# Optimization experiments

Measured on AMD Instinct MI355X. Metric: run time of the kernel, lower is better.

## Reference

```python
import jax, jax.numpy as jnp
import numpy as np

B, S, HID = 1, 2048, 1024
HQ, HKV, D = 16, 8, 64
W = 64          # causal window size (includes self at offset 0)
K = 128         # total neighbors per query: W window + (K-W) random rewires


def setup_inputs() -> dict:
    key = jax.random.key(0)
    ks = jax.random.split(key, 8)
    hidden_states = jax.random.normal(ks[0], (B, S, HID), jnp.float32)
    sc = HID ** -0.5
    q_w = jax.random.normal(ks[1], (HQ * D, HID), jnp.float32) * sc
    k_w = jax.random.normal(ks[2], (HKV * D, HID), jnp.float32) * sc
    v_w = jax.random.normal(ks[3], (HKV * D, HID), jnp.float32) * sc
    o_w = jax.random.normal(ks[4], (HQ * D, HID), jnp.float32).T * sc  # [HID, HQ*D] -> stored as [HID, HQ*D]? keep [HID, HQ*D]
    o_w = jax.random.normal(ks[4], (HID, HQ * D), jnp.float32) * sc
    edge_bias = jax.random.normal(ks[5], (4,), jnp.float32) * 0.1
    # neighbor indices: per kv-head, per query position.
    pos = jnp.arange(S)
    win = pos[:, None] - jnp.arange(W)[None, :]                    # [S, W], offset 0 == self
    win = jnp.broadcast_to(win[None], (HKV, S, W))
    rew = jax.random.randint(ks[6], (HKV, S, K - W), 0, S)         # random rewire edges
    neigh_idx = jnp.concatenate([win, rew], axis=-1).astype(jnp.int32)  # [HKV, S, K]
    edge_type = jnp.concatenate([
        jnp.full((HKV, S, W), 1, jnp.int32),       # 'window'
        jnp.full((HKV, S, K - W), 3, jnp.int32),   # 'rewire'
    ], axis=-1)
    return {
        'hidden_states': hidden_states, 'q_w': q_w, 'k_w': k_w, 'v_w': v_w,
        'o_w': o_w, 'edge_bias': edge_bias, 'neigh_idx': neigh_idx,
        'edge_type': edge_type,
    }


def reference(hidden_states, q_w, k_w, v_w, o_w, edge_bias, neigh_idx, edge_type):
    b, s, _ = hidden_states.shape
    hkv, _, kk = neigh_idx.shape
    hq = q_w.shape[0] // (k_w.shape[0] // hkv)
    d = k_w.shape[0] // hkv
    hq = q_w.shape[0] // d
    g = hq // hkv
    scaling = d ** -0.5

    # projections (nn.Linear: x @ W.T)
    q = (hidden_states @ q_w.T).reshape(b, s, hq, d).transpose(0, 2, 1, 3)    # [B,HQ,S,D]
    k = (hidden_states @ k_w.T).reshape(b, s, hkv, d).transpose(0, 2, 1, 3)   # [B,HKV,S,D]
    v = (hidden_states @ v_w.T).reshape(b, s, hkv, d).transpose(0, 2, 1, 3)

    # causal neighbor mask + safe clamp (mirrors _causal_neighbor_mask / _safe_neighbor_idx)
    pos = jnp.arange(s)
    mask = (neigh_idx >= 0) & (neigh_idx < s) & (neigh_idx <= pos[None, :, None])  # [HKV,S,K]
    safe = jnp.clip(neigh_idx, 0, s - 1)

    # gather K/V at neighbor indices: [B,HKV,S,K,D]
    h_idx = jnp.arange(hkv)[:, None, None]
    k_g = k[:, h_idx, safe, :]
    v_g = v[:, h_idx, safe, :]

    # GQA: group query heads over kv heads
    qg = q.reshape(b, hkv, g, s, d)
    scores = jnp.einsum('bhgsd,bhskd->bhgsk', qg, k_g) * scaling              # [B,HKV,G,S,K]
    scores = scores + edge_bias[edge_type][None, :, None, :, :]
    neg = jnp.finfo(scores.dtype).min
    scores = jnp.where(mask[None, :, None, :, :], scores, neg)
    attn = jax.nn.softmax(scores, axis=-1)

    out = jnp.einsum('bhgsk,bhskd->bhgsd', attn, v_g)                         # [B,HKV,G,S,D]
    out = out.reshape(b, hq, s, d).transpose(0, 2, 1, 3).reshape(b, s, hq * d)
    return out @ o_w.T                                                        # [B,S,HID]
```

## Files before the change

kernel.cpp:

```cpp
#include <hip/hip_runtime.h>
#include <hip/hip_bf16.h>

#define S_LEN 2048
#define HIDDEN 1024

typedef __attribute__((ext_vector_type(4))) float f32x4;
typedef __attribute__((ext_vector_type(8))) _Float16 f16x8;
typedef __attribute__((ext_vector_type(2))) _Float16 f16x2;
typedef __attribute__((ext_vector_type(2))) __fp16 fp16x2;
typedef unsigned short u16;
typedef unsigned int u32;

typedef const __attribute__((address_space(1))) unsigned int as1_u32;
typedef __attribute__((address_space(3))) unsigned int as3_u32;

__device__ __forceinline__ u16 f2h(float f) {
  union { _Float16 h; u16 u; } c; c.h = (_Float16)f; return c.u;
}
__device__ __forceinline__ f16x2 u2h2(u32 u) {
  union { u32 x; f16x2 h; } c; c.x = u; return c.h;
}
__device__ __forceinline__ float fdot2(u32 a, u32 b, float c) {
#if __has_builtin(__builtin_amdgcn_fdot2)
  return __builtin_amdgcn_fdot2(u2h2(a), u2h2(b), c, false);
#else
  f16x2 ha = u2h2(a), hb = u2h2(b);
  return fmaf((float)ha.x, (float)hb.x, fmaf((float)ha.y, (float)hb.y, c));
#endif
}
__device__ __forceinline__ u32 pkrtz(float a, float b) {
#if __has_builtin(__builtin_amdgcn_cvt_pkrtz)
  union { fp16x2 h; u32 u; } c;
  c.h = __builtin_amdgcn_cvt_pkrtz(a, b);
  return c.u;
#else
  union { f16x2 h; u32 u; } c;
  c.h.x = (_Float16)a; c.h.y = (_Float16)b;
  return c.u;
#endif
}

__global__ __launch_bounds__(256) void cvt_all(
    const float* __restrict__ h, const float* __restrict__ qw,
    const float* __restrict__ kw, const float* __restrict__ vw,
    const float* __restrict__ ow, u16* __restrict__ hb, u16* __restrict__ qwb,
    u16* __restrict__ kwb, u16* __restrict__ vwb, u16* __restrict__ owb) {
  const int b = blockIdx.x;
  const float* src; u16* dst; int base;
  if (b < 2048)      { src = h;  dst = hb;  base = b; }
  else if (b < 3072) { src = qw; dst = qwb; base = b - 2048; }
  else if (b < 3584) { src = kw; dst = kwb; base = b - 3072; }
  else if (b < 4096) { src = vw; dst = vwb; base = b - 3584; }
  else               { src = ow; dst = owb; base = b - 4096; }
  const int i = base * 256 + threadIdx.x;
  const float4 v = ((const float4*)src)[i];
  ushort4 r;
  r.x = f2h(v.x); r.y = f2h(v.y); r.z = f2h(v.z); r.w = f2h(v.w);
  ((ushort4*)dst)[i] = r;
}

template <int BM, bool OUT_F16>
__device__ __forceinline__ void gemm_core(
    u16* __restrict__ As, u16* __restrict__ Bs,
    const u16* __restrict__ A, const u16* __restrict__ W, void* __restrict__ Cv,
    int Kd, int ldc, int mtile, int ntile) {
  constexpr int MF = BM / 32;
  const int tid = threadIdx.x;
  const int lane = tid & 63;
  const int wave = tid >> 6;
  const int wr = wave >> 1, wc = wave & 1;
  f32x4 acc[MF][4] = {};
  const int m0 = mtile * BM, n0 = ntile * 128;

  for (int kt = 0; kt < Kd; kt += 32) {
#pragma unroll
    for (int i = 0; i < BM / 64; ++i) {
      const int e = (i * 256 + tid) * 8;
      const int r = e >> 5, c = e & 31;
      __builtin_amdgcn_global_load_lds(
          (as1_u32*)(A + (size_t)(m0 + r) * Kd + kt + c), (as3_u32*)(As + e), 16, 0, 0);
    }
#pragma unroll
    for (int i = 0; i < 2; ++i) {
      const int e = (i * 256 + tid) * 8;
      const int r = e >> 5, c = e & 31;
      __builtin_amdgcn_global_load_lds(
          (as1_u32*)(W + (size_t)(n0 + r) * Kd + kt + c), (as3_u32*)(Bs + e), 16, 0, 0);
    }
    __syncthreads();
    f16x8 af[MF], bfr[4];
#pragma unroll
    for (int mi = 0; mi < MF; ++mi)
      af[mi] = *(const f16x8*)(As + (wr * (BM / 2) + mi * 16 + (lane & 15)) * 32 + (lane >> 4) * 8);
#pragma unroll
    for (int ni = 0; ni < 4; ++ni)
      bfr[ni] = *(const f16x8*)(Bs + (wc * 64 + ni * 16 + (lane & 15)) * 32 + (lane >> 4) * 8);
#pragma unroll
    for (int mi = 0; mi < MF; ++mi)
#pragma unroll
      for (int ni = 0; ni < 4; ++ni)
        acc[mi][ni] = __builtin_amdgcn_mfma_f32_16x16x32_f16(af[mi], bfr[ni], acc[mi][ni], 0, 0, 0);
    __syncthreads();
  }

#pragma unroll
  for (int mi = 0; mi < MF; ++mi) {
#pragma unroll
    for (int ni = 0; ni < 4; ++ni) {
      const int row0 = m0 + wr * (BM / 2) + mi * 16 + (lane >> 4) * 4;
      const int col = n0 + wc * 64 + ni * 16 + (lane & 15);
#pragma unroll
      for (int r = 0; r < 4; ++r) {
        if (OUT_F16)
          ((u16*)Cv)[(size_t)(row0 + r) * ldc + col] = f2h(acc[mi][ni][r]);
        else
          ((float*)Cv)[(size_t)(row0 + r) * ldc + col] = acc[mi][ni][r];
      }
    }
  }
}

__global__ __launch_bounds__(256, 2) void qkv_gemm(
    const u16* __restrict__ hb, const u16* __restrict__ qwb,
    const u16* __restrict__ kwb, const u16* __restrict__ vwb,
    u16* __restrict__ Qb, u16* __restrict__ Kb, u16* __restrict__ Vb) {
  __shared__ u16 As[128 * 32];
  __shared__ u16 Bs[128 * 32];
  const int nt = blockIdx.x, mt = blockIdx.y;
  if (nt < 8)       gemm_core<128, true>(As, Bs, hb, qwb, Qb, HIDDEN, 1024, mt, nt);
  else if (nt < 12) gemm_core<128, true>(As, Bs, hb, kwb, Kb, HIDDEN, 512, mt, nt - 8);
  else              gemm_core<128, true>(As, Bs, hb, vwb, Vb, HIDDEN, 512, mt, nt - 12);
}

__global__ __launch_bounds__(256, 2) void o_gemm(
    const u16* __restrict__ attnb, const u16* __restrict__ owb,
    float* __restrict__ out) {
  __shared__ u16 As[64 * 32];
  __shared__ u16 Bs[128 * 32];
  gemm_core<64, false>(As, Bs, attnb, owb, out, HIDDEN, 1024, blockIdx.y, blockIdx.x);
}

#define WIN_ROWS 72
#define WIN_ELEMS (WIN_ROWS * 64)
__global__ __launch_bounds__(256, 5) void attn_kernel(
    const u16* __restrict__ Qb, const u16* __restrict__ Kb,
    const u16* __restrict__ Vb, const int* __restrict__ neigh,
    const float* __restrict__ ebias, u16* __restrict__ attnb) {
  __shared__ u16 kwin[WIN_ELEMS];
  __shared__ u16 vwin[WIN_ELEMS];
  __shared__ u32 park[4][192];

  const int tid = threadIdx.x;
  const int lane = tid & 63;
  const int wv = tid >> 6;
  const int h = blockIdx.y;
  const int s0 = blockIdx.x * 4;
  const int s = s0 + wv;

  const u16* Kp = Kb + h * 64;
  const u16* Vp = Vb + h * 64;

  const int iB = neigh[((size_t)h * S_LEN + s) * 128 + 64 + lane];
  const bool okB = (iB >= 0) && (iB <= s);
  const int gB = min(max(iB, 0), S_LEN - 1);
  const bool okA = lane <= s;

  const u16* krp = Kp + (size_t)gB * 512;
  uint4 krreg[8];
#pragma unroll
  for (int t = 0; t < 8; ++t) krreg[t] = *(const uint4*)(krp + t * 8);

  const int chunk = (lane & 7) ^ (lane >> 3);
#pragma unroll
  for (int gg = 0; gg < 2; ++gg) {
    const int g = wv + gg * 4;
    const int r_lds = g * 8 + (lane >> 3);
    const int row = min(max(s0 - 63 + r_lds, 0), S_LEN - 1);
    __builtin_amdgcn_global_load_lds(
        (as1_u32*)(Kp + (size_t)row * 512 + chunk * 8),
        (as3_u32*)(kwin + g * 512 + lane * 8), 16, 0, 0);
    __builtin_amdgcn_global_load_lds(
        (as1_u32*)(Vp + (size_t)row * 512 + chunk * 8),
        (as3_u32*)(vwin + g * 512 + lane * 8), 16, 0, 0);
  }
  if (wv == 0) {
    const int g = 8;
    const int r_lds = g * 8 + (lane >> 3);
    const int row = min(max(s0 - 63 + r_lds, 0), S_LEN - 1);
    __builtin_amdgcn_global_load_lds(
        (as1_u32*)(Kp + (size_t)row * 512 + chunk * 8),
        (as3_u32*)(kwin + g * 512 + lane * 8), 16, 0, 0);
    __builtin_amdgcn_global_load_lds(
        (as1_u32*)(Vp + (size_t)row * 512 + chunk * 8),
        (as3_u32*)(vwin + g * 512 + lane * 8), 16, 0, 0);
  }

  __syncthreads();

  const u16* qp = Qb + (size_t)s * 1024 + h * 128;
  const int rW = wv + 63 - lane;
  const u16* kwrow = kwin + rW * 64;
  const int rw7 = rW & 7;
  float sA0 = 0.f, sA1 = 0.f, sB0 = 0.f, sB1 = 0.f;
#pragma unroll
  for (int t = 0; t < 8; ++t) {
    const uint4 kw = *(const uint4*)(kwrow + ((t ^ rw7) << 3));
    const uint4 kr = krreg[t];
    const uint4 qa = *(const uint4*)(qp + t * 8);
    const uint4 qb = *(const uint4*)(qp + 64 + t * 8);
    sA0 = fdot2(kw.x, qa.x, sA0); sA0 = fdot2(kw.y, qa.y, sA0);
    sA0 = fdot2(kw.z, qa.z, sA0); sA0 = fdot2(kw.w, qa.w, sA0);
    sA1 = fdot2(kw.x, qb.x, sA1); sA1 = fdot2(kw.y, qb.y, sA1);
    sA1 = fdot2(kw.z, qb.z, sA1); sA1 = fdot2(kw.w, qb.w, sA1);
    sB0 = fdot2(kr.x, qa.x, sB0); sB0 = fdot2(kr.y, qa.y, sB0);
    sB0 = fdot2(kr.z, qa.z, sB0); sB0 = fdot2(kr.w, qa.w, sB0);
    sB1 = fdot2(kr.x, qb.x, sB1); sB1 = fdot2(kr.y, qb.y, sB1);
    sB1 = fdot2(kr.z, qb.z, sB1); sB1 = fdot2(kr.w, qb.w, sB1);
  }

  const float NEG = -1e30f;
  const float SC = 0.125f;
  const float ebW = ebias[1];
  const float ebR = ebias[3];
  sA0 = okA ? fmaf(sA0, SC, ebW) : NEG;
  sA1 = okA ? fmaf(sA1, SC, ebW) : NEG;
  sB0 = okB ? fmaf(sB0, SC, ebR) : NEG;
  sB1 = okB ? fmaf(sB1, SC, ebR) : NEG;

  float m0 = fmaxf(sA0, sB0), m1 = fmaxf(sA1, sB1);
#pragma unroll
  for (int off = 32; off; off >>= 1) {
    m0 = fmaxf(m0, __shfl_xor(m0, off));
    m1 = fmaxf(m1, __shfl_xor(m1, off));
  }
  float eA0 = __expf(sA0 - m0), eB0 = __expf(sB0 - m0);
  float eA1 = __expf(sA1 - m1), eB1 = __expf(sB1 - m1);
  float d0 = eA0 + eB0, d1 = eA1 + eB1;
#pragma unroll
  for (int off = 32; off; off >>= 1) {
    d0 += __shfl_xor(d0, off);
    d1 += __shfl_xor(d1, off);
  }
  const float rc0 = 1.0f / d0, rc1 = 1.0f / d1;

  u32* pb = park[wv];
  int* ib = (int*)(park[wv] + 128);
  const float pA0 = eA0 * rc0, pA1 = eA1 * rc1;
  const float pB0 = eB0 * rc0, pB1 = eB1 * rc1;
  const float hA0 = __shfl_xor(pA0, 1), hA1 = __shfl_xor(pA1, 1);
  const float hB0 = __shfl_xor(pB0, 1), hB1 = __shfl_xor(pB1, 1);
  ib[lane] = gB;
  if (!(lane & 1)) {
    uint4 pk;
    pk.x = pkrtz(pA0, hA0);
    pk.y = pkrtz(pA1, hA1);
    pk.z = pkrtz(pB0, hB0);
    pk.w = pkrtz(pB1, hB1);
    *(uint4*)(pb + (lane >> 1) * 4) = pk;
  }
  asm volatile("s_waitcnt lgkmcnt(0)" ::: "memory");

  float a0 = 0.f, a1 = 0.f;
  const int ln7 = lane & 7, lnc = lane >> 3;
#pragma unroll 4
  for (int m = 0; m < 32; ++m) {
    const uint4 pp = *(const uint4*)(pb + m * 4);
    const int2 rB = *(const int2*)(ib + m * 2);
    const int rl0 = wv + 63 - 2 * m;
    const int rl1 = rl0 - 1;
    const int a0i = (rl0 >> 3) * 512 + ((rl0 & 7) * 8 + (lnc ^ (rl0 & 7))) * 8 + ln7;
    const int a1i = (rl1 >> 3) * 512 + ((rl1 & 7) * 8 + (lnc ^ (rl1 & 7))) * 8 + ln7;
    const u32 w0 = vwin[a0i];
    const u32 w1 = vwin[a1i];
    const u32 b0 = Vp[(size_t)rB.x * 512 + lane];
    const u32 b1 = Vp[(size_t)rB.y * 512 + lane];
    const u32 wpair = (w1 << 16) | w0;
    const u32 bpair = (b1 << 16) | b0;
    a0 = fdot2(wpair, pp.x, a0);
    a1 = fdot2(wpair, pp.y, a1);
    a0 = fdot2(bpair, pp.z, a0);
    a1 = fdot2(bpair, pp.w, a1);
  }

  u16* op = attnb + (size_t)s * 1024 + h * 128;
  op[lane] = f2h(a0);
  op[64 + lane] = f2h(a1);
}

extern "C" void kernel_launch(void* const* d_in, const int* in_sizes, int n_in,
                              void* d_out, int out_size, void* d_ws, size_t ws_size,
                              hipStream_t stream) {
  const float* hidden = (const float*)d_in[0];
  const float* q_w = (const float*)d_in[1];
  const float* k_w = (const float*)d_in[2];
  const float* v_w = (const float*)d_in[3];
  const float* o_w = (const float*)d_in[4];
  const float* ebias = (const float*)d_in[5];
  const int* neigh = (const int*)d_in[6];
  float* out = (float*)d_out;

  char* ws = (char*)d_ws;
  u16* hb    = (u16*)(ws + (0ull << 20));
  u16* qwb   = (u16*)(ws + (4ull << 20));
  u16* kwb   = (u16*)(ws + (6ull << 20));
  u16* vwb   = (u16*)(ws + (7ull << 20));
  u16* owb   = (u16*)(ws + (8ull << 20));
  u16* Qb    = (u16*)(ws + (10ull << 20));
  u16* Kb    = (u16*)(ws + (14ull << 20));
  u16* Vb    = (u16*)(ws + (16ull << 20));
  u16* attnb = (u16*)(ws + (18ull << 20));

  cvt_all<<<5120, 256, 0, stream>>>(hidden, q_w, k_w, v_w, o_w,
                                    hb, qwb, kwb, vwb, owb);
  qkv_gemm<<<dim3(16, 16), 256, 0, stream>>>(hb, qwb, kwb, vwb, Qb, Kb, Vb);
  attn_kernel<<<dim3(512, 8), 256, 0, stream>>>(Qb, Kb, Vb, neigh, ebias, attnb);
  o_gemm<<<dim3(8, 32), 256, 0, stream>>>(attnb, owb, out);
}
```

Measured before the change: 95.21 us.

## Double-buffer GEMM LDS tiles and store attention V window transposed as packed pairs

The shared GEMM core now double-buffers its A/B LDS tiles, issuing the next k-slice's global-to-LDS loads before computing on the current one, so load latency overlaps MFMA work. In the attention kernel the V window is loaded through registers into a transposed, padded LDS layout of packed f16 pairs. The PV loop can then read a ready-made pair (or align two words for odd waves) instead of two scalar swizzled LDS reads and a shift/or. In exchange, GEMM LDS usage doubles, which may cut occupancy, and the V window load becomes synchronous register loads rather than async LDS DMA.

```diff
diff --git a/kernel.cpp b/kernel.cpp
--- a/kernel.cpp
+++ b/kernel.cpp
@@ -37,6 +37,13 @@
   union { f16x2 h; u32 u; } c;
   c.h.x = (_Float16)a; c.h.y = (_Float16)b;
   return c.u;
+#endif
+}
+__device__ __forceinline__ u32 alignbit16(u32 hi, u32 lo) {
+#if __has_builtin(__builtin_amdgcn_alignbit)
+  return __builtin_amdgcn_alignbit(hi, lo, 16);
+#else
+  return (hi << 16) | (lo >> 16);
 #endif
 }
 
@@ -71,36 +78,48 @@
   const int wr = wave >> 1, wc = wave & 1;
   f32x4 acc[MF][4] = {};
   const int m0 = mtile * BM, n0 = ntile * 128;
-
-  for (int kt = 0; kt < Kd; kt += 32) {
+  const int nk = Kd >> 5;
+
+  auto stage = [&](int buf, int kt) {
+    u16* Ad = As + buf * (BM * 32);
+    u16* Bd = Bs + buf * (128 * 32);
 #pragma unroll
     for (int i = 0; i < BM / 64; ++i) {
       const int e = (i * 256 + tid) * 8;
       const int r = e >> 5, c = e & 31;
       __builtin_amdgcn_global_load_lds(
-          (as1_u32*)(A + (size_t)(m0 + r) * Kd + kt + c), (as3_u32*)(As + e), 16, 0, 0);
+          (as1_u32*)(A + (size_t)(m0 + r) * Kd + kt * 32 + c), (as3_u32*)(Ad + e), 16, 0, 0);
     }
 #pragma unroll
     for (int i = 0; i < 2; ++i) {
       const int e = (i * 256 + tid) * 8;
       const int r = e >> 5, c = e & 31;
       __builtin_amdgcn_global_load_lds(
-          (as1_u32*)(W + (size_t)(n0 + r) * Kd + kt + c), (as3_u32*)(Bs + e), 16, 0, 0);
+          (as1_u32*)(W + (size_t)(n0 + r) * Kd + kt * 32 + c), (as3_u32*)(Bd + e), 16, 0, 0);
     }
-    __syncthreads();
+  };
+
+  stage(0, 0);
+  __syncthreads();
+  int cur = 0;
+  for (int kt = 0; kt < nk; ++kt) {
+    if (kt + 1 < nk) stage(cur ^ 1, kt + 1);
+    const u16* Ac = As + cur * (BM * 32);
+    const u16* Bc = Bs + cur * (128 * 32);
     f16x8 af[MF], bfr[4];
 #pragma unroll
     for (int mi = 0; mi < MF; ++mi)
-      af[mi] = *(const f16x8*)(As + (wr * (BM / 2) + mi * 16 + (lane & 15)) * 32 + (lane >> 4) * 8);
+      af[mi] = *(const f16x8*)(Ac + (wr * (BM / 2) + mi * 16 + (lane & 15)) * 32 + (lane >> 4) * 8);
 #pragma unroll
     for (int ni = 0; ni < 4; ++ni)
-      bfr[ni] = *(const f16x8*)(Bs + (wc * 64 + ni * 16 + (lane & 15)) * 32 + (lane >> 4) * 8);
+      bfr[ni] = *(const f16x8*)(Bc + (wc * 64 + ni * 16 + (lane & 15)) * 32 + (lane >> 4) * 8);
 #pragma unroll
     for (int mi = 0; mi < MF; ++mi)
 #pragma unroll
       for (int ni = 0; ni < 4; ++ni)
         acc[mi][ni] = __builtin_amdgcn_mfma_f32_16x16x32_f16(af[mi], bfr[ni], acc[mi][ni], 0, 0, 0);
     __syncthreads();
+    cur ^= 1;
   }
 
 #pragma unroll
@@ -124,8 +143,8 @@
     const u16* __restrict__ hb, const u16* __restrict__ qwb,
     const u16* __restrict__ kwb, const u16* __restrict__ vwb,
     u16* __restrict__ Qb, u16* __restrict__ Kb, u16* __restrict__ Vb) {
-  __shared__ u16 As[128 * 32];
-  __shared__ u16 Bs[128 * 32];
+  __shared__ u16 As[2 * 128 * 32];
+  __shared__ u16 Bs[2 * 128 * 32];
   const int nt = blockIdx.x, mt = blockIdx.y;
   if (nt < 8)       gemm_core<128, true>(As, Bs, hb, qwb, Qb, HIDDEN, 1024, mt, nt);
   else if (nt < 12) gemm_core<128, true>(As, Bs, hb, kwb, Kb, HIDDEN, 512, mt, nt - 8);
@@ -135,19 +154,20 @@
 __global__ __launch_bounds__(256, 2) void o_gemm(
     const u16* __restrict__ attnb, const u16* __restrict__ owb,
     float* __restrict__ out) {
-  __shared__ u16 As[64 * 32];
-  __shared__ u16 Bs[128 * 32];
+  __shared__ u16 As[2 * 64 * 32];
+  __shared__ u16 Bs[2 * 128 * 32];
   gemm_core<64, false>(As, Bs, attnb, owb, out, HIDDEN, 1024, blockIdx.y, blockIdx.x);
 }
 
 #define WIN_ROWS 72
 #define WIN_ELEMS (WIN_ROWS * 64)
+#define VT_LD 41
 __global__ __launch_bounds__(256, 5) void attn_kernel(
     const u16* __restrict__ Qb, const u16* __restrict__ Kb,
     const u16* __restrict__ Vb, const int* __restrict__ neigh,
     const float* __restrict__ ebias, u16* __restrict__ attnb) {
   __shared__ u16 kwin[WIN_ELEMS];
-  __shared__ u16 vwin[WIN_ELEMS];
+  __shared__ u32 vwinT[64 * VT_LD];
   __shared__ u32 park[4][192];
 
   const int tid = threadIdx.x;
@@ -179,9 +199,6 @@
     __builtin_amdgcn_global_load_lds(
         (as1_u32*)(Kp + (size_t)row * 512 + chunk * 8),
         (as3_u32*)(kwin + g * 512 + lane * 8), 16, 0, 0);
-    __builtin_amdgcn_global_load_lds(
-        (as1_u32*)(Vp + (size_t)row * 512 + chunk * 8),
-        (as3_u32*)(vwin + g * 512 + lane * 8), 16, 0, 0);
   }
   if (wv == 0) {
     const int g = 8;
@@ -190,9 +207,17 @@
     __builtin_amdgcn_global_load_lds(
         (as1_u32*)(Kp + (size_t)row * 512 + chunk * 8),
         (as3_u32*)(kwin + g * 512 + lane * 8), 16, 0, 0);
-    __builtin_amdgcn_global_load_lds(
-        (as1_u32*)(Vp + (size_t)row * 512 + chunk * 8),
-        (as3_u32*)(vwin + g * 512 + lane * 8), 16, 0, 0);
+  }
+
+#pragma unroll
+  for (int t = 0; t < 9; ++t) {
+    const int k = wv + 4 * t;
+    const int i0r = 2 * k;
+    const int g0 = min(max(s0 - 63 + i0r, 0), S_LEN - 1);
+    const int g1 = min(max(s0 - 62 + i0r, 0), S_LEN - 1);
+    const u32 w0 = Vp[(size_t)g0 * 512 + lane];
+    const u32 w1 = Vp[(size_t)g1 * 512 + lane];
+    vwinT[lane * VT_LD + k] = (w1 << 16) | w0;
   }
 
   __syncthreads();
@@ -252,8 +277,8 @@
   ib[lane] = gB;
   if (!(lane & 1)) {
     uint4 pk;
-    pk.x = pkrtz(pA0, hA0);
-    pk.y = pkrtz(pA1, hA1);
+    pk.x = pkrtz(hA0, pA0);
+    pk.y = pkrtz(hA1, pA1);
     pk.z = pkrtz(pB0, hB0);
     pk.w = pkrtz(pB1, hB1);
     *(uint4*)(pb + (lane >> 1) * 4) = pk;
@@ -261,20 +286,23 @@
   asm volatile("s_waitcnt lgkmcnt(0)" ::: "memory");
 
   float a0 = 0.f, a1 = 0.f;
-  const int ln7 = lane & 7, lnc = lane >> 3;
-#pragma unroll 4
+  const u32* vtr = vwinT + lane * VT_LD;
+  const int keven = (wv >> 1) + 31;
+  const int kodd = ((wv + 63) >> 1);
+#pragma unroll
   for (int m = 0; m < 32; ++m) {
     const uint4 pp = *(const uint4*)(pb + m * 4);
     const int2 rB = *(const int2*)(ib + m * 2);
-    const int rl0 = wv + 63 - 2 * m;
-    const int rl1 = rl0 - 1;
-    const int a0i = (rl0 >> 3) * 512 + ((rl0 & 7) * 8 + (lnc ^ (rl0 & 7))) * 8 + ln7;
-    const int a1i = (rl1 >> 3) * 512 + ((rl1 & 7) * 8 + (lnc ^ (rl1 & 7))) * 8 + ln7;
-    const u32 w0 = vwin[a0i];
-    const u32 w1 = vwin[a1i];
+    u32 wpair;
+    if ((wv & 1) == 0) {
+      wpair = vtr[keven - m];
+    } else {
+      const u32 lo = vtr[kodd - 1 - m];
+      const u32 hi = vtr[kodd - m];
+      wpair = alignbit16(hi, lo);
+    }
     const u32 b0 = Vp[(size_t)rB.x * 512 + lane];
     const u32 b1 = Vp[(size_t)rB.y * 512 + lane];
-    const u32 wpair = (w1 << 16) | w0;
     const u32 bpair = (b1 << 16) | b0;
     a0 = fdot2(wpair, pp.x, a0);
     a1 = fdot2(wpair, pp.y, a1);
```

After: 255.7 us. 169% more time.
